# Kernel optimization log

Hardware: AMD Instinct MI355X
Metric: run time of the kernel (lower is better)

Reference implementation:

```python
import jax, jax.numpy as jnp
import numpy as np

B, T, C = 16, 4000, 512
H, K = 8, 31
PAD, STRIDE, DIL = 15, 1, 1


def setup_inputs() -> dict:
    key = jax.random.key(0)
    k1, k2 = jax.random.split(key, 2)
    x = jax.random.normal(k1, (B, T, C), jnp.float32)
    # xavier_uniform on (H, 1, K): fan_in = 1*K, fan_out = 1*K -> limit = sqrt(6/(2K))
    limit = float(np.sqrt(6.0 / (2.0 * K)))
    weights = jax.random.uniform(k2, (H, 1, K), jnp.float32, -limit, limit)
    bias_weights = jnp.zeros((H,), jnp.float32)
    return {"x": x, "weights": weights, "bias_weights": bias_weights}


def reference(x, weights, bias_weights):
    # softmax-normalized per-head kernel (weight_dropout=0 -> eval identity)
    w = jax.nn.softmax(weights, axis=-1)                # (H, 1, K)
    # torch reshape (B,C,T)->(B*C/H, H, T) maps channel c to head c % H;
    # tile replicates heads in exactly that order -> kernel per channel.
    w_full = jnp.tile(w, (C // H, 1, 1))                 # (C, 1, K)
    xc = jnp.transpose(x, (0, 2, 1))                     # (B, C, T)
    out = jax.lax.conv_general_dilated(
        xc, w_full,
        window_strides=(STRIDE,),
        padding=[(PAD, PAD)],
        rhs_dilation=(DIL,),
        feature_group_count=C,
        dimension_numbers=("NCH", "OIH", "NCH"))        # (B, C, T)
    b_full = jnp.tile(bias_weights, C // H)              # (C,) bias per head -> per channel
    out = out + b_full[None, :, None]
    return jnp.transpose(out, (0, 2, 1))                 # (B, T, C)
```

## Files before the change

### kernel.cpp

```cpp
#include <hip/hip_runtime.h>
#include <math.h>


constexpr int NB   = 16;
constexpr int NT   = 4000;
constexpr int NC   = 512;
constexpr int NH   = 8;
constexpr int NK   = 31;
constexpr int CPAD = 15;

constexpr int SEG  = 80;
constexpr int CH   = 16;
constexpr int HALO = NK - 1;
constexpr int WIN  = CH + HALO;

__global__ __launch_bounds__(512) void lconv_kernel(
    const float* __restrict__ x,
    const float* __restrict__ w,
    const float* __restrict__ bias,
    float* __restrict__ out)
{
    const int c  = threadIdx.x;
    const int b  = blockIdx.y;
    const int t0 = blockIdx.x * SEG;
    const int h  = c & (NH - 1);

    float wr[NK];
    #pragma unroll
    for (int k = 0; k < NK; ++k) wr[k] = w[h * NK + k];
    float m = wr[0];
    #pragma unroll
    for (int k = 1; k < NK; ++k) m = fmaxf(m, wr[k]);
    float s = 0.0f;
    #pragma unroll
    for (int k = 0; k < NK; ++k) { wr[k] = __expf(wr[k] - m); s += wr[k]; }
    const float inv = 1.0f / s;
    #pragma unroll
    for (int k = 0; k < NK; ++k) wr[k] *= inv;
    const float bv = bias[h];

    const float* xb = x   + (size_t)b * NT * NC + c;
    float*       ob = out + (size_t)b * NT * NC + c;

    float win[WIN];

    #pragma unroll
    for (int i = 0; i < HALO; ++i) {
        const int t = t0 - CPAD + i;
        win[i] = (t >= 0) ? xb[(size_t)t * NC] : 0.0f;
    }

    #pragma unroll 1
    for (int tc = t0; tc < t0 + SEG; tc += CH) {
        #pragma unroll
        for (int j = 0; j < CH; ++j) {
            const int t = tc + CPAD + j;
            win[HALO + j] = (t < NT) ? xb[(size_t)t * NC] : 0.0f;
        }
        #pragma unroll
        for (int j = 0; j < CH; ++j) {
            float acc = bv;
            #pragma unroll
            for (int k = 0; k < NK; ++k) acc = fmaf(win[j + k], wr[k], acc);
            ob[(size_t)(tc + j) * NC] = acc;
        }
        #pragma unroll
        for (int i = 0; i < HALO; ++i) win[i] = win[i + CH];
    }
}

extern "C" void kernel_launch(void* const* d_in, const int* in_sizes, int n_in,
                              void* d_out, int out_size, void* d_ws, size_t ws_size,
                              hipStream_t stream) {
    const float* x    = (const float*)d_in[0];
    const float* w    = (const float*)d_in[1];
    const float* bias = (const float*)d_in[2];
    float*       out  = (float*)d_out;

    dim3 grid(NT / SEG, NB);
    lconv_kernel<<<grid, 512, 0, stream>>>(x, w, bias, out);
}
```

Measured before the change: 244.3 us.

## Precompute softmax weights in separate kernel and shrink per-block time segment

Moves the per-thread softmax of the conv weights into a tiny one-block kernel that writes normalized weights to workspace. The main kernel now covers one 16-step chunk per block with 256 channels, on a 3D grid with many more, smaller blocks. Each block loads its full 46-row window in one go, with an unguarded fast path for interior chunks. This drops the redundant exp work and the register shifting between chunks and raises parallelism. In exchange, the halo is re-read more often (46 rows loaded per 16 outputs versus about 30 per 16 before) and there is an extra kernel launch.

```diff
diff --git a/kernel.cpp b/kernel.cpp
--- a/kernel.cpp
+++ b/kernel.cpp
@@ -9,63 +9,65 @@
 constexpr int NK   = 31;
 constexpr int CPAD = 15;
 
-constexpr int SEG  = 80;
 constexpr int CH   = 16;
 constexpr int HALO = NK - 1;
 constexpr int WIN  = CH + HALO;
 
-__global__ __launch_bounds__(512) void lconv_kernel(
+__global__ __launch_bounds__(64) void softmax_w_kernel(
+    const float* __restrict__ w, float* __restrict__ wn)
+{
+    const int h = threadIdx.x;
+    if (h >= NH) return;
+    float v[NK];
+    float m = -1e30f;
+    #pragma unroll
+    for (int k = 0; k < NK; ++k) { v[k] = w[h * NK + k]; m = fmaxf(m, v[k]); }
+    float s = 0.0f;
+    #pragma unroll
+    for (int k = 0; k < NK; ++k) { v[k] = __expf(v[k] - m); s += v[k]; }
+    const float inv = 1.0f / s;
+    #pragma unroll
+    for (int k = 0; k < NK; ++k) wn[h * NK + k] = v[k] * inv;
+}
+
+__global__ __launch_bounds__(256, 4) void lconv_kernel(
     const float* __restrict__ x,
-    const float* __restrict__ w,
+    const float* __restrict__ wn,
     const float* __restrict__ bias,
     float* __restrict__ out)
 {
-    const int c  = threadIdx.x;
-    const int b  = blockIdx.y;
-    const int t0 = blockIdx.x * SEG;
+    const int c  = blockIdx.y * 256 + threadIdx.x;
+    const int b  = blockIdx.z;
+    const int t0 = blockIdx.x * CH;
     const int h  = c & (NH - 1);
-
-    float wr[NK];
-    #pragma unroll
-    for (int k = 0; k < NK; ++k) wr[k] = w[h * NK + k];
-    float m = wr[0];
-    #pragma unroll
-    for (int k = 1; k < NK; ++k) m = fmaxf(m, wr[k]);
-    float s = 0.0f;
-    #pragma unroll
-    for (int k = 0; k < NK; ++k) { wr[k] = __expf(wr[k] - m); s += wr[k]; }
-    const float inv = 1.0f / s;
-    #pragma unroll
-    for (int k = 0; k < NK; ++k) wr[k] *= inv;
-    const float bv = bias[h];
 
     const float* xb = x   + (size_t)b * NT * NC + c;
     float*       ob = out + (size_t)b * NT * NC + c;
 
+    float wr[NK];
+    #pragma unroll
+    for (int k = 0; k < NK; ++k) wr[k] = wn[h * NK + k];
+    const float bv = bias[h];
+
     float win[WIN];
+    if (t0 >= CPAD && t0 + CH - 1 + CPAD < NT) {
+        #pragma unroll
+        for (int i = 0; i < WIN; ++i)
+            win[i] = xb[(size_t)(t0 - CPAD + i) * NC];
+    } else {
+        #pragma unroll
+        for (int i = 0; i < WIN; ++i) {
+            const int t = t0 - CPAD + i;
+            win[i] = (t >= 0 && t < NT) ? xb[(size_t)t * NC] : 0.0f;
+        }
+    }
 
     #pragma unroll
-    for (int i = 0; i < HALO; ++i) {
-        const int t = t0 - CPAD + i;
-        win[i] = (t >= 0) ? xb[(size_t)t * NC] : 0.0f;
-    }
-
-    #pragma unroll 1
-    for (int tc = t0; tc < t0 + SEG; tc += CH) {
+    for (int j = 0; j < CH; ++j) {
+        float acc = bv;
         #pragma unroll
-        for (int j = 0; j < CH; ++j) {
-            const int t = tc + CPAD + j;
-            win[HALO + j] = (t < NT) ? xb[(size_t)t * NC] : 0.0f;
-        }
-        #pragma unroll
-        for (int j = 0; j < CH; ++j) {
-            float acc = bv;
-            #pragma unroll
-            for (int k = 0; k < NK; ++k) acc = fmaf(win[j + k], wr[k], acc);
-            ob[(size_t)(tc + j) * NC] = acc;
-        }
-        #pragma unroll
-        for (int i = 0; i < HALO; ++i) win[i] = win[i + CH];
+        for (int k = 0; k < NK; ++k) acc = fmaf(win[j + k], wr[k], acc);
+        ob[(size_t)(t0 + j) * NC] = acc;
     }
 }
 
@@ -76,7 +78,9 @@
     const float* w    = (const float*)d_in[1];
     const float* bias = (const float*)d_in[2];
     float*       out  = (float*)d_out;
+    float*       wnrm = (float*)d_ws;
 
-    dim3 grid(NT / SEG, NB);
-    lconv_kernel<<<grid, 512, 0, stream>>>(x, w, bias, out);
+    softmax_w_kernel<<<1, 64, 0, stream>>>(w, wnrm);
+    dim3 grid(NT / CH, NC / 256, NB);
+    lconv_kernel<<<grid, 256, 0, stream>>>(x, wnrm, bias, out);
 }
```

Result: faster. 236.4 us (-3.3%).
